# Kernel optimization log

Hardware: AMD Instinct MI355X
Metric: run time of the kernel (lower is better)

Reference implementation:

```python
import jax, jax.numpy as jnp
import numpy as np

N, K, CARD = 8192, 64, 64
LAMBDA = 0.1
BIG = 1e9  # stand-in for +inf that stays finite under fp32


def setup_inputs() -> dict:
    key = jax.random.key(0)
    k1, k2, k3, k4, k5, k6 = jax.random.split(key, 6)
    adj = jax.random.uniform(k1, (N, N), dtype=jnp.float32)
    adj = 0.5 * (adj + adj.T)  # symmetric weighted adjacency
    soft_label = jax.nn.softmax(jax.random.normal(k2, (N, K), dtype=jnp.float32), axis=-1)

    def mk_dgm(k):
        # ground-truth persistence diagram: (card, 2) with birth <= death in [0,1]
        return jnp.sort(jax.random.uniform(k, (CARD, 2), dtype=jnp.float32), axis=-1)

    return {
        "adj": adj,
        "soft_label": soft_label,
        "dgm_gt_b0": mk_dgm(k3),
        "dgm_gt_b1": mk_dgm(k4),
        "dgm_gt_n0": mk_dgm(k5),
        "dgm_gt_n1": mk_dgm(k6),
    }


def community_distance(adj, S):
    # build_community_graph: C = S^T A S (KxK community graph), turn weights
    # into a sublevel filtration distance D = 1 - C/max(C) (weight-rank style).
    C = S.T @ (adj @ S)                      # [K,K]
    C = 0.5 * (C + C.T)
    C = C / (jnp.max(C) + 1e-12)
    D = 1.0 - C
    Kn = D.shape[0]
    return D.at[jnp.diag_indices(Kn)].set(0.0)


def prim_mst(D):
    # Prim's MST over the complete K-node graph; differentiable w.r.t. D via
    # gathered edge weights (argmin indices are piecewise-constant).
    Kn = D.shape[0]
    in_tree0 = jnp.zeros(Kn, dtype=bool).at[0].set(True)

    def step(in_tree, _):
        masked = jnp.where(in_tree[:, None] & (~in_tree)[None, :], D, BIG)
        idx = jnp.argmin(masked)
        u, v = idx // Kn, idx % Kn
        return in_tree.at[v].set(True), (D[u, v], u, v)

    _, (ws, us, vs) = jax.lax.scan(step, in_tree0, None, length=Kn - 1)
    return ws, us, vs


def dgm_dim0(ws):
    # dim-0 pairs: every vertex born at 0, dies at the MST edge merging it.
    # keep_essential_parts=False drops the infinite bar. Pad/sort to CARD.
    pad = CARD - ws.shape[0]
    deaths = jax.lax.top_k(jnp.concatenate([ws, jnp.zeros(pad, ws.dtype)]), CARD)[0]
    return jnp.stack([jnp.zeros(CARD, ws.dtype), deaths], axis=-1)  # [CARD,2]


def dgm_dim1(D, us, vs):
    # dim-1 pairs of the clique (Rips) filtration: each non-MST edge (i,j)
    # births a 1-cycle at D[i,j]; its death is approximated by the cheapest
    # triangle filling it: min_k max(D[i,j], D[i,k], D[j,k]).
    Kn = D.shape[0]
    mst = jnp.zeros((Kn, Kn), dtype=bool).at[us, vs].set(True)
    mst = mst | mst.T
    # M[i,j,k] = filtration value of triangle (i,j,k)
    M = jnp.maximum(D[:, :, None], jnp.maximum(D[:, None, :], D[None, :, :]))
    kk = jnp.arange(Kn)
    bad = (kk[None, None, :] == kk[:, None, None]) | (kk[None, None, :] == kk[None, :, None])
    death = jnp.min(jnp.where(bad, BIG, M), axis=-1)     # [K,K]
    valid = jnp.triu(jnp.ones((Kn, Kn), dtype=bool), 1) & (~mst)
    pers = jnp.where(valid, death - D, -1.0)
    top_p, top_idx = jax.lax.top_k(pers.reshape(-1), CARD)
    b = jnp.take(D.reshape(-1), top_idx)
    d = jnp.take(death.reshape(-1), top_idx)
    keep = top_p > 0
    return jnp.stack([jnp.where(keep, b, 0.0), jnp.where(keep, d, 0.0)], axis=-1)


def wasserstein_w1(X, Y, eps=0.01, iters=300):
    # 1-Wasserstein diagram distance (internal_p = inf), with diagonal
    # projections as an extra sink row/column; solved by entropic Sinkhorn.
    n, m = X.shape[0], Y.shape[0]
    Cxy = jnp.max(jnp.abs(X[:, None, :] - Y[None, :, :]), axis=-1)  # [n,m]
    dX = 0.5 * (X[:, 1] - X[:, 0])  # L_inf distance to diagonal
    dY = 0.5 * (Y[:, 1] - Y[:, 0])
    C = jnp.zeros((n + 1, m + 1), X.dtype).at[:n, :m].set(Cxy).at[:n, m].set(dX).at[n, :m].set(dY)
    loga = jnp.log(jnp.concatenate([jnp.ones(n), jnp.full((1,), float(m))]))
    logb = jnp.log(jnp.concatenate([jnp.ones(m), jnp.full((1,), float(n))]))

    def step(fg, _):
        f, g = fg
        f = eps * (loga - jax.nn.logsumexp((g[None, :] - C) / eps, axis=1))
        g = eps * (logb - jax.nn.logsumexp((f[:, None] - C) / eps, axis=0))
        return (f, g), None

    (f, g), _ = jax.lax.scan(step, (jnp.zeros(n + 1), jnp.zeros(m + 1)), None, length=iters)
    P = jnp.exp((f[:, None] + g[None, :] - C) / eps)
    return jnp.sum(P * C)


def reference(adj, soft_label, dgm_gt_b0, dgm_gt_b1, dgm_gt_n0, dgm_gt_n1):
    D = community_distance(adj, soft_label)
    ws, us, vs = prim_mst(D)
    dgm0 = dgm_dim0(ws)
    dgm1 = dgm_dim1(D, us, vs)
    loss = (wasserstein_w1(dgm0, dgm_gt_b0) + wasserstein_w1(dgm1, dgm_gt_b1)
            + wasserstein_w1(dgm0, dgm_gt_n0) + wasserstein_w1(dgm1, dgm_gt_n1))
    return LAMBDA * loss
```

## Files before the change

kernel.cpp:

```cpp
#include <hip/hip_runtime.h>
#include <hip/hip_bf16.h>

#define NN 8192
#define KK 64
#define CARD 64
#define AST_OFF   0
#define CRAW_OFF  524288
#define DGM0_OFF  528384
#define DGM1_OFF  528512

__device__ __forceinline__ double rdlane(double x, int l) {
  int lo = __builtin_amdgcn_readlane(__double2loint(x), l);
  int hi = __builtin_amdgcn_readlane(__double2hiint(x), l);
  return __hiloint2double(hi, lo);
}
__device__ __forceinline__ double bflysum(double x) {
#pragma unroll
  for (int o = 32; o > 0; o >>= 1) x += __shfl_xor(x, o);
  return x;
}

#define KSPLIT 16
#define KT 32
#define RB 256
__global__ __launch_bounds__(256, 2) void k_gemm_as(
    const float* __restrict__ A, const float* __restrict__ S,
    float* __restrict__ AST) {
  __shared__ float At[KT][RB + 1];
  __shared__ float Sl[KT][64];
  const int tid = threadIdx.x;
  const int rb = blockIdx.x >> 4;
  const int ks = blockIdx.x & 15;
  const int r0 = rb * RB;
  const int lane = tid & 63;
  const int cg = __builtin_amdgcn_readfirstlane(tid >> 6);
  const int c0 = cg * 16;

  float acc[4][16];
#pragma unroll
  for (int r = 0; r < 4; ++r)
#pragma unroll
    for (int q = 0; q < 16; ++q) acc[r][q] = 0.0f;

  const int kbeg = ks * (NN / KSPLIT);
  for (int kt = kbeg; kt < kbeg + NN / KSPLIT; kt += KT) {
#pragma unroll
    for (int p = 0; p < 8; ++p) {
      int fi = p * 256 + tid;
      int rr = fi >> 3, cc = (fi & 7) * 4;
      float4 v = *reinterpret_cast<const float4*>(
          A + (size_t)(r0 + rr) * NN + kt + cc);
      At[cc + 0][rr] = v.x; At[cc + 1][rr] = v.y;
      At[cc + 2][rr] = v.z; At[cc + 3][rr] = v.w;
    }
#pragma unroll
    for (int p = 0; p < 2; ++p) {
      int fi = p * 256 + tid;
      int rr = fi >> 4, cc = (fi & 15) * 4;
      float4 v = *reinterpret_cast<const float4*>(
          S + (size_t)(kt + rr) * KK + cc);
      *reinterpret_cast<float4*>(&Sl[rr][cc]) = v;
    }
    __syncthreads();
#pragma unroll 2
    for (int k = 0; k < KT; ++k) {
      float a0 = At[k][lane];
      float a1 = At[k][lane + 64];
      float a2 = At[k][lane + 128];
      float a3 = At[k][lane + 192];
      const float4* Sv = reinterpret_cast<const float4*>(&Sl[k][c0]);
      float4 s0 = Sv[0], s1 = Sv[1], s2 = Sv[2], s3 = Sv[3];
      float sc[16] = {s0.x, s0.y, s0.z, s0.w, s1.x, s1.y, s1.z, s1.w,
                      s2.x, s2.y, s2.z, s2.w, s3.x, s3.y, s3.z, s3.w};
#pragma unroll
      for (int q = 0; q < 16; ++q) {
        acc[0][q] = fmaf(a0, sc[q], acc[0][q]);
        acc[1][q] = fmaf(a1, sc[q], acc[1][q]);
        acc[2][q] = fmaf(a2, sc[q], acc[2][q]);
        acc[3][q] = fmaf(a3, sc[q], acc[3][q]);
      }
    }
    __syncthreads();
  }
#pragma unroll
  for (int r = 0; r < 4; ++r)
#pragma unroll
    for (int q = 0; q < 16; ++q)
      unsafeAtomicAdd(&AST[(size_t)(c0 + q) * NN + r0 + r * 64 + lane],
                      acc[r][q]);
}

__global__ __launch_bounds__(256) void k_gemm_c(
    const float* __restrict__ S, const float* __restrict__ AST,
    float* __restrict__ CRAW) {
  const int j = blockIdx.x & 63;
  const int iseg = blockIdx.x >> 6;
  const int lane = threadIdx.x & 63;
  const int s4 = __builtin_amdgcn_readfirstlane(threadIdx.x >> 6);
  const int i0 = iseg * 1024 + s4 * 256;
  const float* astj = AST + (size_t)j * NN + i0;
  float acc = 0.0f;
  for (int i = 0; i < 256; i += 4) {
    float4 a4 = *reinterpret_cast<const float4*>(astj + i);
    const float* Srow = S + (size_t)(i0 + i) * KK + lane;
    acc = fmaf(a4.x, Srow[0 * KK], acc);
    acc = fmaf(a4.y, Srow[1 * KK], acc);
    acc = fmaf(a4.z, Srow[2 * KK], acc);
    acc = fmaf(a4.w, Srow[3 * KK], acc);
  }
  __shared__ float red[4][64];
  red[s4][lane] = acc;
  __syncthreads();
  if (threadIdx.x < 64) {
    unsafeAtomicAdd(&CRAW[j * 64 + lane],
                    red[0][lane] + red[1][lane] + red[2][lane] + red[3][lane]);
  }
}

__global__ __launch_bounds__(256) void k_topo(
    const float* __restrict__ CRAW, float* __restrict__ DGM0,
    float* __restrict__ DGM1, float* __restrict__ out) {
  __shared__ float Dl[64 * 66];
  __shared__ float red[4];
  __shared__ float wsE[64];
  __shared__ int usE[64], vsE[64];
  __shared__ unsigned char msk[4096];
  __shared__ float death[4096];
  __shared__ float pers[4096];
  __shared__ float rv[4];
  __shared__ int ri[4];
  const int t = threadIdx.x;

  if (t == 0) out[0] = 0.0f;

  float lmax = -1e30f;
#pragma unroll
  for (int m = 0; m < 16; ++m) {
    int idx = t + 256 * m;
    int a = idx >> 6, b = idx & 63;
    float v = 0.5f * (CRAW[idx] + CRAW[b * 64 + a]);
    Dl[a * 66 + b] = v;
    lmax = fmaxf(lmax, v);
  }
  for (int o = 32; o > 0; o >>= 1) lmax = fmaxf(lmax, __shfl_xor(lmax, o));
  if ((t & 63) == 0) red[t >> 6] = lmax;
  __syncthreads();
  const float mx = fmaxf(fmaxf(red[0], red[1]), fmaxf(red[2], red[3]));
  const float inv = 1.0f / (mx + 1e-12f);
  __syncthreads();
#pragma unroll
  for (int m = 0; m < 16; ++m) {
    int idx = t + 256 * m;
    int a = idx >> 6, b = idx & 63;
    float v = 1.0f - Dl[a * 66 + b] * inv;
    Dl[a * 66 + b] = (a == b) ? 0.0f : v;
  }
  __syncthreads();

  if (t < 64) {
    const int lane = t;
    bool intree = (lane == 0);
    float key = Dl[0 * 66 + lane];
    int par = 0;
    for (int step = 0; step < 63; ++step) {
      float kv = intree ? 1e9f : key;
      int ki = lane;
      for (int o = 32; o > 0; o >>= 1) {
        float ov = __shfl_xor(kv, o);
        int oi = __shfl_xor(ki, o);
        if (ov < kv || (ov == kv && oi < ki)) { kv = ov; ki = oi; }
      }
      int pu = __shfl(par, ki);
      if (lane == 0) { wsE[step] = kv; usE[step] = pu; vsE[step] = ki; }
      if (lane == ki) intree = true;
      float dn = Dl[ki * 66 + lane];
      if (!intree && dn < key) { key = dn; par = ki; }
    }
  }
  __syncthreads();

  for (int idx = t; idx < 4096; idx += 256) msk[idx] = 0;
  __syncthreads();
  if (t < 63) {
    int u = usE[t], v = vsE[t];
    msk[u * 64 + v] = 1;
    msk[v * 64 + u] = 1;
  }
  __syncthreads();

  if (t < 64) {
    float wv = (t < 63) ? wsE[t] : 0.0f;
    int rank = 0;
    for (int o = 0; o < 64; ++o) {
      float wo = (o < 63) ? wsE[o] : 0.0f;
      rank += (wo > wv) || (wo == wv && o < t);
    }
    DGM0[rank * 2 + 0] = 0.0f;
    DGM0[rank * 2 + 1] = wv;
  }

  for (int p = t; p < 4096; p += 256) {
    int i = p >> 6, j = p & 63;
    float dij = Dl[i * 66 + j];
    float tmin = 1e9f;
#pragma unroll 8
    for (int k2 = 0; k2 < 64; ++k2) {
      float m2 = fmaxf(Dl[i * 66 + k2], Dl[j * 66 + k2]);
      tmin = fminf(tmin, (k2 == i || k2 == j) ? 1e9f : m2);
    }
    float de = fmaxf(dij, tmin);
    death[p] = de;
    bool valid = (j > i) && (!msk[p]);
    pers[p] = valid ? (de - dij) : -1.0f;
  }
  __syncthreads();

  for (int r = 0; r < 64; ++r) {
    float bv = -1e30f;
    int bi = 0;
    for (int p = t; p < 4096; p += 256) {
      float v = pers[p];
      if (v > bv) { bv = v; bi = p; }
    }
    for (int o = 32; o > 0; o >>= 1) {
      float ov = __shfl_xor(bv, o);
      int oi = __shfl_xor(bi, o);
      if (ov > bv || (ov == bv && oi < bi)) { bv = ov; bi = oi; }
    }
    if ((t & 63) == 0) { rv[t >> 6] = bv; ri[t >> 6] = bi; }
    __syncthreads();
    if (t == 0) {
      for (int q = 1; q < 4; ++q)
        if (rv[q] > bv || (rv[q] == bv && ri[q] < bi)) { bv = rv[q]; bi = ri[q]; }
      bool keep = bv > 0.0f;
      int i = bi >> 6, j = bi & 63;
      DGM1[r * 2 + 0] = keep ? Dl[i * 66 + j] : 0.0f;
      DGM1[r * 2 + 1] = keep ? death[bi] : 0.0f;
      pers[bi] = -3.0f;
    }
    __syncthreads();
  }
}

typedef double d4 __attribute__((ext_vector_type(4)));

__global__ __launch_bounds__(64) void k_sinkhorn(
    const float* __restrict__ DGM0, const float* __restrict__ DGM1,
    const float* __restrict__ G0, const float* __restrict__ G1,
    const float* __restrict__ G2, const float* __restrict__ G3,
    float* __restrict__ out) {
  const int b = blockIdx.x;
  const float* X = (b & 1) ? DGM1 : DGM0;
  const float* Y = (b == 0) ? G0 : (b == 1) ? G1 : (b == 2) ? G2 : G3;

  __shared__ float Cf[65][66];
  __shared__ double Wd[65][66];

  const int lane = threadIdx.x;
  const float INVE = 100.0f;

  for (int idx = lane; idx < 65 * 65; idx += 64) {
    int i = idx / 65, j = idx - i * 65;
    float cv;
    if (i < 64) {
      float xb = X[i * 2], xd = X[i * 2 + 1];
      if (j < 64)
        cv = fmaxf(fabsf(xb - Y[j * 2]), fabsf(xd - Y[j * 2 + 1]));
      else
        cv = 0.5f * (xd - xb);
    } else {
      cv = (j < 64) ? 0.5f * (Y[j * 2 + 1] - Y[j * 2]) : 0.0f;
    }
    Cf[i][j] = cv * INVE;
  }
  __syncthreads();
  for (int idx = lane; idx < 65 * 65; idx += 64) {
    int i = idx / 65, j = idx - i * 65;
    Wd[i][j] = exp(-(double)Cf[i][j]);
  }
  __syncthreads();

  d4 F0, F1, F2, F3, F4, F5, F6, F7, F8, F9, F10, F11, F12, F13, F14, F15;
#define LOADF(n)                   \
  {                                \
    F##n.x = Wd[lane][4 * n + 0];  \
    F##n.y = Wd[lane][4 * n + 1];  \
    F##n.z = Wd[lane][4 * n + 2];  \
    F##n.w = Wd[lane][4 * n + 3];  \
  }
  LOADF(0) LOADF(1) LOADF(2) LOADF(3) LOADF(4) LOADF(5) LOADF(6) LOADF(7)
  LOADF(8) LOADF(9) LOADF(10) LOADF(11) LOADF(12) LOADF(13) LOADF(14)
  LOADF(15)
  const double WF8 = Wd[lane][64];
  const double W64r = Wd[64][lane];

  double u = 1.0, v = 1.0, u64 = 1.0, v64 = 1.0;

#define USTEP(n)                                \
  {                                             \
    a0 = fma(F##n.x, rdlane(v, 4 * n + 0), a0); \
    a1 = fma(F##n.y, rdlane(v, 4 * n + 1), a1); \
    a2 = fma(F##n.z, rdlane(v, 4 * n + 2), a2); \
    a3 = fma(F##n.w, rdlane(v, 4 * n + 3), a3); \
  }
#define VSTEP(n)                                             \
  {                                                          \
    b0 = fma(Wd[4 * n + 0][lane], rdlane(u, 4 * n + 0), b0); \
    b1 = fma(Wd[4 * n + 1][lane], rdlane(u, 4 * n + 1), b1); \
    b2 = fma(Wd[4 * n + 2][lane], rdlane(u, 4 * n + 2), b2); \
    b3 = fma(Wd[4 * n + 3][lane], rdlane(u, 4 * n + 3), b3); \
  }

  for (int it = 0; it < 300; ++it) {
    double t64 = bflysum(W64r * v);

    double a0 = 0.0, a1 = 0.0, a2 = 0.0, a3 = 0.0;
    USTEP(0) USTEP(1) USTEP(2) USTEP(3) USTEP(4) USTEP(5) USTEP(6) USTEP(7)
    USTEP(8) USTEP(9) USTEP(10) USTEP(11) USTEP(12) USTEP(13) USTEP(14)
    USTEP(15)
    double s = ((a0 + a1) + (a2 + a3)) + WF8 * v64;
    u = 1.0 / s;
    u64 = 64.0 / (t64 + v64);

    double t8 = bflysum(WF8 * u);

    double b0 = 0.0, b1 = 0.0, b2 = 0.0, b3 = 0.0;
    VSTEP(0) VSTEP(1) VSTEP(2) VSTEP(3) VSTEP(4) VSTEP(5) VSTEP(6) VSTEP(7)
    VSTEP(8) VSTEP(9) VSTEP(10) VSTEP(11) VSTEP(12) VSTEP(13) VSTEP(14)
    VSTEP(15)
    double sv = ((b0 + b1) + (b2 + b3)) + W64r * u64;
    v = 1.0 / sv;
    v64 = 64.0 / (t8 + u64);
  }

  double acc = 0.0;
#define LSTEP(n)                                                            \
  {                                                                         \
    acc += u * F##n.x * rdlane(v, 4 * n + 0) * (double)Cf[lane][4 * n + 0]; \
    acc += u * F##n.y * rdlane(v, 4 * n + 1) * (double)Cf[lane][4 * n + 1]; \
    acc += u * F##n.z * rdlane(v, 4 * n + 2) * (double)Cf[lane][4 * n + 2]; \
    acc += u * F##n.w * rdlane(v, 4 * n + 3) * (double)Cf[lane][4 * n + 3]; \
  }
  LSTEP(0) LSTEP(1) LSTEP(2) LSTEP(3) LSTEP(4) LSTEP(5) LSTEP(6) LSTEP(7)
  LSTEP(8) LSTEP(9) LSTEP(10) LSTEP(11) LSTEP(12) LSTEP(13) LSTEP(14)
  LSTEP(15)
  acc += u * WF8 * v64 * (double)Cf[lane][64];
  acc += u64 * W64r * v * (double)Cf[64][lane];
  float af = (float)acc;
#pragma unroll
  for (int o = 32; o > 0; o >>= 1) af += __shfl_xor(af, o);
  if (lane == 0)
    atomicAdd(out, 0.1f * 0.01f * af);
}

extern "C" void kernel_launch(void* const* d_in, const int* in_sizes, int n_in,
                              void* d_out, int out_size, void* d_ws,
                              size_t ws_size, hipStream_t stream) {
  const float* A = (const float*)d_in[0];
  const float* S = (const float*)d_in[1];
  const float* G0 = (const float*)d_in[2];
  const float* G1 = (const float*)d_in[3];
  const float* G2 = (const float*)d_in[4];
  const float* G3 = (const float*)d_in[5];
  float* out = (float*)d_out;
  float* ws = (float*)d_ws;

  float* AST = ws + AST_OFF;
  float* CRAW = ws + CRAW_OFF;
  float* DGM0 = ws + DGM0_OFF;
  float* DGM1 = ws + DGM1_OFF;

  (void)hipMemsetAsync(AST, 0, (size_t)(64 * NN + 64 * 64) * sizeof(float),
                       stream);

  k_gemm_as<<<dim3(32 * KSPLIT), dim3(256), 0, stream>>>(A, S, AST);
  k_gemm_c<<<dim3(64 * 8), dim3(256), 0, stream>>>(S, AST, CRAW);
  k_topo<<<dim3(1), dim3(256), 0, stream>>>(CRAW, DGM0, DGM1, out);
  k_sinkhorn<<<dim3(4), dim3(64), 0, stream>>>(DGM0, DGM1, G0, G1, G2, G3,
                                               out);
}
```

Before: 1.117 ms.

## Split Sinkhorn matvecs across two wavefronts with register-resident kernel columns

The Sinkhorn kernel now runs 128 threads per block, so each of two wavefronts handles half of the 64 columns in the u- and v-updates. Partial sums are exchanged through small shared arrays with a block barrier after each half-step. The transposed kernel is also held in registers (Gc) instead of being reread from a shared double array every iteration, and the shared Wd buffer is removed. This halves the serial FMA/readlane chain per iteration, but adds two __syncthreads and shared-memory round trips to each of the 300 iterations.

```diff
diff --git a/kernel.cpp b/kernel.cpp
--- a/kernel.cpp
+++ b/kernel.cpp
@@ -244,7 +244,7 @@
 
 typedef double d4 __attribute__((ext_vector_type(4)));
 
-__global__ __launch_bounds__(64) void k_sinkhorn(
+__global__ __launch_bounds__(128) void k_sinkhorn(
     const float* __restrict__ DGM0, const float* __restrict__ DGM1,
     const float* __restrict__ G0, const float* __restrict__ G1,
     const float* __restrict__ G2, const float* __restrict__ G3,
@@ -254,12 +254,16 @@
   const float* Y = (b == 0) ? G0 : (b == 1) ? G1 : (b == 2) ? G2 : G3;
 
   __shared__ float Cf[65][66];
-  __shared__ double Wd[65][66];
-
-  const int lane = threadIdx.x;
+  __shared__ double pmu[2][66];
+  __shared__ double pmv[2][66];
+
+  const int t = threadIdx.x;
+  const int lane = t & 63;
+  const int w = __builtin_amdgcn_readfirstlane(t >> 6);
+  const int base = 32 * w;
   const float INVE = 100.0f;
 
-  for (int idx = lane; idx < 65 * 65; idx += 64) {
+  for (int idx = t; idx < 65 * 65; idx += 128) {
     int i = idx / 65, j = idx - i * 65;
     float cv;
     if (i < 64) {
@@ -274,41 +278,43 @@
     Cf[i][j] = cv * INVE;
   }
   __syncthreads();
-  for (int idx = lane; idx < 65 * 65; idx += 64) {
-    int i = idx / 65, j = idx - i * 65;
-    Wd[i][j] = exp(-(double)Cf[i][j]);
-  }
-  __syncthreads();
-
-  d4 F0, F1, F2, F3, F4, F5, F6, F7, F8, F9, F10, F11, F12, F13, F14, F15;
-#define LOADF(n)                   \
-  {                                \
-    F##n.x = Wd[lane][4 * n + 0];  \
-    F##n.y = Wd[lane][4 * n + 1];  \
-    F##n.z = Wd[lane][4 * n + 2];  \
-    F##n.w = Wd[lane][4 * n + 3];  \
+
+  d4 F0, F1, F2, F3, F4, F5, F6, F7;
+  d4 Gc0, Gc1, Gc2, Gc3, Gc4, Gc5, Gc6, Gc7;
+#define LOADF(n)                                         \
+  {                                                      \
+    F##n.x = exp(-(double)Cf[lane][base + 4 * n + 0]);   \
+    F##n.y = exp(-(double)Cf[lane][base + 4 * n + 1]);   \
+    F##n.z = exp(-(double)Cf[lane][base + 4 * n + 2]);   \
+    F##n.w = exp(-(double)Cf[lane][base + 4 * n + 3]);   \
+  }
+#define LOADG(n)                                         \
+  {                                                      \
+    Gc##n.x = exp(-(double)Cf[base + 4 * n + 0][lane]);  \
+    Gc##n.y = exp(-(double)Cf[base + 4 * n + 1][lane]);  \
+    Gc##n.z = exp(-(double)Cf[base + 4 * n + 2][lane]);  \
+    Gc##n.w = exp(-(double)Cf[base + 4 * n + 3][lane]);  \
   }
   LOADF(0) LOADF(1) LOADF(2) LOADF(3) LOADF(4) LOADF(5) LOADF(6) LOADF(7)
-  LOADF(8) LOADF(9) LOADF(10) LOADF(11) LOADF(12) LOADF(13) LOADF(14)
-  LOADF(15)
-  const double WF8 = Wd[lane][64];
-  const double W64r = Wd[64][lane];
+  LOADG(0) LOADG(1) LOADG(2) LOADG(3) LOADG(4) LOADG(5) LOADG(6) LOADG(7)
+  const double WF8 = exp(-(double)Cf[lane][64]);
+  const double W64r = exp(-(double)Cf[64][lane]);
 
   double u = 1.0, v = 1.0, u64 = 1.0, v64 = 1.0;
 
-#define USTEP(n)                                \
-  {                                             \
-    a0 = fma(F##n.x, rdlane(v, 4 * n + 0), a0); \
-    a1 = fma(F##n.y, rdlane(v, 4 * n + 1), a1); \
-    a2 = fma(F##n.z, rdlane(v, 4 * n + 2), a2); \
-    a3 = fma(F##n.w, rdlane(v, 4 * n + 3), a3); \
-  }
-#define VSTEP(n)                                             \
-  {                                                          \
-    b0 = fma(Wd[4 * n + 0][lane], rdlane(u, 4 * n + 0), b0); \
-    b1 = fma(Wd[4 * n + 1][lane], rdlane(u, 4 * n + 1), b1); \
-    b2 = fma(Wd[4 * n + 2][lane], rdlane(u, 4 * n + 2), b2); \
-    b3 = fma(Wd[4 * n + 3][lane], rdlane(u, 4 * n + 3), b3); \
+#define USTEP(n)                                       \
+  {                                                    \
+    a0 = fma(F##n.x, rdlane(v, base + 4 * n + 0), a0); \
+    a1 = fma(F##n.y, rdlane(v, base + 4 * n + 1), a1); \
+    a2 = fma(F##n.z, rdlane(v, base + 4 * n + 2), a2); \
+    a3 = fma(F##n.w, rdlane(v, base + 4 * n + 3), a3); \
+  }
+#define VSTEP(n)                                        \
+  {                                                     \
+    b0 = fma(Gc##n.x, rdlane(u, base + 4 * n + 0), b0); \
+    b1 = fma(Gc##n.y, rdlane(u, base + 4 * n + 1), b1); \
+    b2 = fma(Gc##n.z, rdlane(u, base + 4 * n + 2), b2); \
+    b3 = fma(Gc##n.w, rdlane(u, base + 4 * n + 3), b3); \
   }
 
   for (int it = 0; it < 300; ++it) {
@@ -316,9 +322,9 @@
 
     double a0 = 0.0, a1 = 0.0, a2 = 0.0, a3 = 0.0;
     USTEP(0) USTEP(1) USTEP(2) USTEP(3) USTEP(4) USTEP(5) USTEP(6) USTEP(7)
-    USTEP(8) USTEP(9) USTEP(10) USTEP(11) USTEP(12) USTEP(13) USTEP(14)
-    USTEP(15)
-    double s = ((a0 + a1) + (a2 + a3)) + WF8 * v64;
+    pmu[w][lane] = (a0 + a1) + (a2 + a3);
+    __syncthreads();
+    double s = pmu[0][lane] + pmu[1][lane] + WF8 * v64;
     u = 1.0 / s;
     u64 = 64.0 / (t64 + v64);
 
@@ -326,26 +332,30 @@
 
     double b0 = 0.0, b1 = 0.0, b2 = 0.0, b3 = 0.0;
     VSTEP(0) VSTEP(1) VSTEP(2) VSTEP(3) VSTEP(4) VSTEP(5) VSTEP(6) VSTEP(7)
-    VSTEP(8) VSTEP(9) VSTEP(10) VSTEP(11) VSTEP(12) VSTEP(13) VSTEP(14)
-    VSTEP(15)
-    double sv = ((b0 + b1) + (b2 + b3)) + W64r * u64;
+    pmv[w][lane] = (b0 + b1) + (b2 + b3);
+    __syncthreads();
+    double sv = pmv[0][lane] + pmv[1][lane] + W64r * u64;
     v = 1.0 / sv;
     v64 = 64.0 / (t8 + u64);
   }
 
   double acc = 0.0;
-#define LSTEP(n)                                                            \
-  {                                                                         \
-    acc += u * F##n.x * rdlane(v, 4 * n + 0) * (double)Cf[lane][4 * n + 0]; \
-    acc += u * F##n.y * rdlane(v, 4 * n + 1) * (double)Cf[lane][4 * n + 1]; \
-    acc += u * F##n.z * rdlane(v, 4 * n + 2) * (double)Cf[lane][4 * n + 2]; \
-    acc += u * F##n.w * rdlane(v, 4 * n + 3) * (double)Cf[lane][4 * n + 3]; \
+#define LSTEP(n)                                               \
+  {                                                            \
+    acc += u * F##n.x * rdlane(v, base + 4 * n + 0) *          \
+           (double)Cf[lane][base + 4 * n + 0];                 \
+    acc += u * F##n.y * rdlane(v, base + 4 * n + 1) *          \
+           (double)Cf[lane][base + 4 * n + 1];                 \
+    acc += u * F##n.z * rdlane(v, base + 4 * n + 2) *          \
+           (double)Cf[lane][base + 4 * n + 2];                 \
+    acc += u * F##n.w * rdlane(v, base + 4 * n + 3) *          \
+           (double)Cf[lane][base + 4 * n + 3];                 \
   }
   LSTEP(0) LSTEP(1) LSTEP(2) LSTEP(3) LSTEP(4) LSTEP(5) LSTEP(6) LSTEP(7)
-  LSTEP(8) LSTEP(9) LSTEP(10) LSTEP(11) LSTEP(12) LSTEP(13) LSTEP(14)
-  LSTEP(15)
-  acc += u * WF8 * v64 * (double)Cf[lane][64];
-  acc += u64 * W64r * v * (double)Cf[64][lane];
+  if (w == 0)
+    acc += u * WF8 * v64 * (double)Cf[lane][64];
+  else
+    acc += u64 * W64r * v * (double)Cf[64][lane];
   float af = (float)acc;
 #pragma unroll
   for (int o = 32; o > 0; o >>= 1) af += __shfl_xor(af, o);
@@ -376,6 +386,6 @@
   k_gemm_as<<<dim3(32 * KSPLIT), dim3(256), 0, stream>>>(A, S, AST);
   k_gemm_c<<<dim3(64 * 8), dim3(256), 0, stream>>>(S, AST, CRAW);
   k_topo<<<dim3(1), dim3(256), 0, stream>>>(CRAW, DGM0, DGM1, out);
-  k_sinkhorn<<<dim3(4), dim3(64), 0, stream>>>(DGM0, DGM1, G0, G1, G2, G3,
-                                               out);
-}
+  k_sinkhorn<<<dim3(4), dim3(128), 0, stream>>>(DGM0, DGM1, G0, G1, G2, G3,
+                                                out);
+}
```

Result: faster. 1.075 ms (-3.8%).
